# Kernel optimization log

Hardware: AMD Instinct MI355X
Metric: run time of the kernel (lower is better)

## Reference

```python
import jax, jax.numpy as jnp
import numpy as np

B, NP, K, E = 8, 4096, 1024, 262144   # graphs, nodes/graph, topk keep, edges
N = B * NP
EPS = 1e-5


def _glorot(k, fi, fo):
    lim = float(np.sqrt(6.0 / (fi + fo)))
    return jax.random.uniform(k, (fi, fo), jnp.float32, -lim, lim)


def setup_inputs() -> dict:
    key = jax.random.key(0)
    ks = jax.random.split(key, 16)
    pos = jax.random.normal(ks[0], (N, 3), jnp.float32)
    epg = E // B
    src = jax.random.randint(ks[1], (E,), 0, NP)
    dst = jax.random.randint(ks[2], (E,), 0, NP)
    off = jnp.repeat(jnp.arange(B) * NP, epg)   # edges stay within their graph
    edge_index = jnp.stack([src + off, dst + off]).astype(jnp.int32)
    batch = jnp.repeat(jnp.arange(B, dtype=jnp.int32), NP)
    inp = {"pos": pos, "edge_index": edge_index, "batch": batch,
           "p": jax.random.normal(ks[3], (3,), jnp.float32)}
    dims = [3, 64, 128, 128, 256, 512]
    for i in range(5):
        fi, fo = dims[i], dims[i + 1]
        inp[f"W{i+1}"] = _glorot(ks[4 + i], fi, fo)
        inp[f"b{i+1}"] = jnp.zeros((fo,), jnp.float32)
        inp[f"g{i+1}"] = jnp.ones((fo,), jnp.float32)
        inp[f"be{i+1}"] = jnp.zeros((fo,), jnp.float32)
    for i, (fi, fo) in enumerate([(512, 256), (256, 256), (256, 100)]):
        inp[f"fw{i+1}"] = _glorot(ks[9 + i], fi, fo)
        inp[f"fb{i+1}"] = jnp.zeros((fo,), jnp.float32)
    return inp


def _bn(x, g, b):
    # BatchNorm1d in training mode: batch stats over the node dim
    m = jnp.mean(x, 0)
    v = jnp.var(x, 0)
    return (x - m) * jax.lax.rsqrt(v + EPS) * g + b


def _gcn(x, src, dst, ew, W, bb, n):
    # GCNConv with add_self_loops=True, symmetric normalization.
    h = x @ W                                              # [n, out]
    deg = jax.ops.segment_sum(ew, dst, num_segments=n) + 1.0  # +1 self-loop
    dinv = jax.lax.rsqrt(deg)
    norm = dinv[src] * ew * dinv[dst]                      # masked edges -> 0
    agg = jax.ops.segment_sum(h[src] * norm[:, None], dst, num_segments=n)
    return agg + h * (dinv * dinv)[:, None] + bb           # self-loop term + bias


def _forward(pos, p, W1, b1, g1, be1, W2, b2, g2, be2, W3, b3, g3, be3,
             W4, b4, g4, be4, W5, b5, g5, be5, fw1, fb1, fw2, fb2, fw3, fb3,
             edge_index):
    # --- TopKPooling(ratio=1024): projection score, tanh, top-k per graph ---
    s = jnp.tanh(pos @ p / jnp.linalg.norm(p))             # [N]
    vals, idx = jax.lax.top_k(s.reshape(B, NP), K)         # [B,K]
    perm = (idx + (jnp.arange(B) * NP)[:, None]).reshape(-1)
    x = pos[perm] * vals.reshape(-1)[:, None]              # gate kept nodes
    Nn = B * K
    remap = jnp.full((N,), -1, jnp.int32).at[perm].set(jnp.arange(Nn, dtype=jnp.int32))
    src, dst = remap[edge_index[0]], remap[edge_index[1]]
    valid = (src >= 0) & (dst >= 0)
    ew = valid.astype(x.dtype)                             # 0-weight == removed edge
    src = jnp.where(valid, src, 0)
    dst = jnp.where(valid, dst, 0)
    for (W, bb, g, be) in ((W1, b1, g1, be1), (W2, b2, g2, be2),
                           (W3, b3, g3, be3), (W4, b4, g4, be4),
                           (W5, b5, g5, be5)):
        x = jax.nn.relu(_bn(_gcn(x, src, dst, ew, W, bb, Nn), g, be))
    # --- global sum pooling (torch_scatter default reduce='sum') ---
    batch_new = jnp.repeat(jnp.arange(B), K)
    x = jax.ops.segment_sum(x, batch_new, num_segments=B)  # [B,512]
    x = jax.nn.relu(x @ fw1 + fb1)
    x = jax.nn.relu(x @ fw2 + fb2)
    return jax.nn.log_softmax(x @ fw3 + fb3, axis=-1)      # [B,100]


def reference(pos, edge_index, batch, p, W1, b1, g1, be1, W2, b2, g2, be2,
              W3, b3, g3, be3, W4, b4, g4, be4, W5, b5, g5, be5,
              fw1, fb1, fw2, fb2, fw3, fb3):
    del batch  # graph ids are the fixed contiguous layout encoded in B, NP, K
    return _forward(pos, p, W1, b1, g1, be1, W2, b2, g2, be2, W3, b3, g3, be3,
                    W4, b4, g4, be4, W5, b5, g5, be5,
                    fw1, fb1, fw2, fb2, fw3, fb3, edge_index)
```

## Files before the change

kernel.cpp:

```cpp
#include <hip/hip_runtime.h>
#include <math.h>

#define NTOT 32768
#define NPG  4096
#define BGR  8
#define KK   1024
#define NN   8192
#define NE   262144

typedef __attribute__((ext_vector_type(8))) short bf16x8;
typedef __attribute__((ext_vector_type(4))) float f32x4;

static __device__ __forceinline__ unsigned short f2bf(float f) {
    unsigned u = __float_as_uint(f);
    return (unsigned short)((u + 0x7fffu + ((u >> 16) & 1u)) >> 16);
}
static __device__ __forceinline__ float bf2f(unsigned short b) {
    return __uint_as_float(((unsigned)b) << 16);
}

__global__ void k_init(int* remap, int* deg, int* cursor) {
    int i = blockIdx.x * blockDim.x + threadIdx.x;
    if (i < NTOT) remap[i] = -1;
    if (i < NN) { deg[i] = 0; cursor[i] = 0; }
}

__global__ __launch_bounds__(1024) void k_topk2(const float* __restrict__ pos,
                                                const float* __restrict__ p,
                                                int* __restrict__ remap,
                                                float* __restrict__ x0f,
                                                unsigned short* __restrict__ Ab0) {
    __shared__ unsigned skey[NPG];
    __shared__ float sval[NPG];
    __shared__ int hist[256];
    __shared__ int Sarr[256];
    __shared__ int wsum[16];
    __shared__ int s_bin, s_above;

    const int g = blockIdx.x, tid = threadIdx.x;
    const int lane = tid & 63, wid = tid >> 6;
    const float p0 = p[0], p1 = p[1], p2 = p[2];
    const float invn = 1.0f / sqrtf(p0 * p0 + p1 * p1 + p2 * p2);

    for (int i = tid; i < NPG; i += 1024) {
        const float* pp = pos + (size_t)(g * NPG + i) * 3;
        float s = tanhf((pp[0] * p0 + pp[1] * p1 + pp[2] * p2) * invn);
        sval[i] = s;
        unsigned b = __float_as_uint(s);
        skey[i] = (b & 0x80000000u) ? ~b : (b | 0x80000000u);
    }
    __syncthreads();

    unsigned prefix = 0;
    int needed = KK;
    for (int r = 0; r < 4; ++r) {
        const int sh = 24 - 8 * r;
        if (tid < 256) hist[tid] = 0;
        __syncthreads();
        for (int i = tid; i < NPG; i += 1024) {
            unsigned k = skey[i];
            bool act = (r == 0) || ((k >> (sh + 8)) == prefix);
            if (act) atomicAdd(&hist[(k >> sh) & 255u], 1);
        }
        __syncthreads();
        if (wid == 0) {
            int h0 = hist[4 * lane + 0], h1 = hist[4 * lane + 1];
            int h2 = hist[4 * lane + 2], h3 = hist[4 * lane + 3];
            int l3 = h3, l2 = h2 + l3, l1 = h1 + l2, l0 = h0 + l1;
            int t = l0;
            for (int off = 1; off < 64; off <<= 1) {
                int n = __shfl_down(t, off, 64);
                if (lane + off < 64) t += n;
            }
            int hi = t - l0;
            Sarr[4 * lane + 0] = l0 + hi;
            Sarr[4 * lane + 1] = l1 + hi;
            Sarr[4 * lane + 2] = l2 + hi;
            Sarr[4 * lane + 3] = l3 + hi;
        }
        __syncthreads();
        if (tid < 256) {
            int Sb = Sarr[tid];
            int Sb1 = (tid < 255) ? Sarr[tid + 1] : 0;
            if (Sb >= needed && Sb1 < needed) { s_bin = tid; s_above = Sb1; }
        }
        __syncthreads();
        needed -= s_above;
        prefix = (prefix << 8) | (unsigned)s_bin;
        __syncthreads();
    }
    const unsigned Tkey = prefix;
    const int needTies = needed;

    int tiebase = 0, keepbase = 0;
    for (int c = 0; c < 4; ++c) {
        const int i = c * 1024 + tid;
        const unsigned k = skey[i];
        const int tie = (k == Tkey) ? 1 : 0;
        int v = tie;
        for (int off = 1; off < 64; off <<= 1) {
            int n = __shfl_up(v, off, 64);
            if (lane >= off) v += n;
        }
        if (lane == 63) wsum[wid] = v;
        __syncthreads();
        if (wid == 0) {
            int w = (lane < 16) ? wsum[lane] : 0;
            for (int off = 1; off < 16; off <<= 1) {
                int n = __shfl_up(w, off, 64);
                if (lane >= off) w += n;
            }
            if (lane < 16) wsum[lane] = w;
        }
        __syncthreads();
        const int trank = tiebase + v + (wid > 0 ? wsum[wid - 1] : 0) - tie;
        const int ttot = wsum[15];
        const int keep = (k > Tkey) || (tie && trank < needTies);
        __syncthreads();
        int u = keep;
        for (int off = 1; off < 64; off <<= 1) {
            int n = __shfl_up(u, off, 64);
            if (lane >= off) u += n;
        }
        if (lane == 63) wsum[wid] = u;
        __syncthreads();
        if (wid == 0) {
            int w = (lane < 16) ? wsum[lane] : 0;
            for (int off = 1; off < 16; off <<= 1) {
                int n = __shfl_up(w, off, 64);
                if (lane >= off) w += n;
            }
            if (lane < 16) wsum[lane] = w;
        }
        __syncthreads();
        const int kincl = u + (wid > 0 ? wsum[wid - 1] : 0);
        const int ktot = wsum[15];
        if (keep) {
            int nn = g * KK + keepbase + kincl - 1;
            remap[g * NPG + i] = nn;
            float val = sval[i];
            const float* pp = pos + (size_t)(g * NPG + i) * 3;
            float v0 = pp[0] * val, v1 = pp[1] * val, v2 = pp[2] * val;
            x0f[(size_t)nn * 3 + 0] = v0;
            x0f[(size_t)nn * 3 + 1] = v1;
            x0f[(size_t)nn * 3 + 2] = v2;
            unsigned short* rw = Ab0 + (size_t)nn * 32;
            ushort4 a = make_ushort4(f2bf(v0), f2bf(v1), f2bf(v2), 0);
            ushort4 z = make_ushort4(0, 0, 0, 0);
            *(ushort4*)(rw) = a;
#pragma unroll
            for (int t = 1; t < 8; ++t) *(ushort4*)(rw + 4 * t) = z;
        }
        tiebase += ttot;
        keepbase += ktot;
        __syncthreads();
    }
}

__global__ void k_deg(const int* __restrict__ ei, const int* __restrict__ remap,
                      int* __restrict__ deg) {
    int e = blockIdx.x * blockDim.x + threadIdx.x;
    if (e >= NE) return;
    int s = remap[ei[e]];
    int d = remap[ei[NE + e]];
    if (s >= 0 && d >= 0) atomicAdd(&deg[d], 1);
}

__global__ __launch_bounds__(1024) void k_scan(const int* __restrict__ deg,
                                               int* __restrict__ rowptr) {
    __shared__ int part[1024];
    const int tid = threadIdx.x;
    const int base = tid * 8;
    int loc[8];
    int s = 0;
#pragma unroll
    for (int i = 0; i < 8; ++i) { loc[i] = s; s += deg[base + i]; }
    part[tid] = s;
    __syncthreads();
    for (int off = 1; off < 1024; off <<= 1) {
        int v = (tid >= off) ? part[tid - off] : 0;
        __syncthreads();
        part[tid] += v;
        __syncthreads();
    }
    int pre = (tid > 0) ? part[tid - 1] : 0;
#pragma unroll
    for (int i = 0; i < 8; ++i) rowptr[base + i] = pre + loc[i];
    if (tid == 1023) rowptr[NN] = pre + s;
}

__global__ void k_place2(const int* __restrict__ ei, const int* __restrict__ remap,
                         const int* __restrict__ deg, const int* __restrict__ rowptr,
                         int* __restrict__ cursor, int* __restrict__ col,
                         float* __restrict__ ew) {
    int e = blockIdx.x * blockDim.x + threadIdx.x;
    if (e >= NE) return;
    int s = remap[ei[e]];
    int d = remap[ei[NE + e]];
    if (s >= 0 && d >= 0) {
        int pos = rowptr[d] + atomicAdd(&cursor[d], 1);
        col[pos] = s;
        ew[pos] = rsqrtf((float)(deg[s] + 1)) * rsqrtf((float)(deg[d] + 1));
    }
}

__global__ void k_wt_all(const float* __restrict__ w0, const float* __restrict__ w1,
                         const float* __restrict__ w2, const float* __restrict__ w3,
                         const float* __restrict__ w4,
                         unsigned short* __restrict__ t0, unsigned short* __restrict__ t1,
                         unsigned short* __restrict__ t2, unsigned short* __restrict__ t3,
                         unsigned short* __restrict__ t4) {
    int i = blockIdx.x * blockDim.x + threadIdx.x;
    const float* W; unsigned short* T; int Kd, Nc, Kpad, base;
    if (i < 2048)        { W = w0; T = t0; Kd = 3;   Nc = 64;  Kpad = 32;  base = 0; }
    else if (i < 10240)  { W = w1; T = t1; Kd = 64;  Nc = 128; Kpad = 64;  base = 2048; }
    else if (i < 26624)  { W = w2; T = t2; Kd = 128; Nc = 128; Kpad = 128; base = 10240; }
    else if (i < 59392)  { W = w3; T = t3; Kd = 128; Nc = 256; Kpad = 128; base = 26624; }
    else if (i < 190464) { W = w4; T = t4; Kd = 256; Nc = 512; Kpad = 256; base = 59392; }
    else return;
    int j = i - base;
    int n = j / Kpad, k = j - n * Kpad;
    float v = (k < Kd) ? W[(size_t)k * Nc + n] : 0.0f;
    T[j] = f2bf(v);
}

__global__ __launch_bounds__(256) void k_mm2(const unsigned short* __restrict__ Ab,
                                             const float* __restrict__ Yin,
                                             const float* __restrict__ scale,
                                             const float* __restrict__ shift,
                                             const unsigned short* __restrict__ WT,
                                             unsigned short* __restrict__ Hb,
                                             int Kd, int Nc) {
    const int lane = threadIdx.x & 63, wid = threadIdx.x >> 6;
    const int bm = blockIdx.x * 64 + (wid >> 1) * 32;
    const int bn = blockIdx.y * 64 + (wid & 1) * 32;
    const int fr = lane & 15;
    const int ko = (lane >> 4) << 3;
    const int row0 = bm + fr;
    const unsigned short* B0 = WT + (size_t)(bn + fr) * Kd + ko;
    const size_t strA = (size_t)16 * Kd;
    f32x4 acc00 = {0,0,0,0}, acc01 = {0,0,0,0}, acc10 = {0,0,0,0}, acc11 = {0,0,0,0};
    for (int k0 = 0; k0 < Kd; k0 += 32) {
        bf16x8 a0, a1;
        if (Yin) {
            const int cc = ko + k0;
            const float4 sc0 = *(const float4*)&scale[cc];
            const float4 sc1 = *(const float4*)&scale[cc + 4];
            const float4 sh0 = *(const float4*)&shift[cc];
            const float4 sh1 = *(const float4*)&shift[cc + 4];
            const float* y0 = Yin + (size_t)row0 * Kd + cc;
            const float* y1 = y0 + strA;
#pragma unroll
            for (int h = 0; h < 2; ++h) {
                const float* yy = h ? y1 : y0;
                float4 u = *(const float4*)yy;
                float4 v = *(const float4*)(yy + 4);
                float r0 = fmaxf(u.x * sc0.x + sh0.x, 0.0f);
                float r1 = fmaxf(u.y * sc0.y + sh0.y, 0.0f);
                float r2 = fmaxf(u.z * sc0.z + sh0.z, 0.0f);
                float r3 = fmaxf(u.w * sc0.w + sh0.w, 0.0f);
                float r4 = fmaxf(v.x * sc1.x + sh1.x, 0.0f);
                float r5 = fmaxf(v.y * sc1.y + sh1.y, 0.0f);
                float r6 = fmaxf(v.z * sc1.z + sh1.z, 0.0f);
                float r7 = fmaxf(v.w * sc1.w + sh1.w, 0.0f);
                bf16x8 a;
                a[0] = (short)f2bf(r0); a[1] = (short)f2bf(r1);
                a[2] = (short)f2bf(r2); a[3] = (short)f2bf(r3);
                a[4] = (short)f2bf(r4); a[5] = (short)f2bf(r5);
                a[6] = (short)f2bf(r6); a[7] = (short)f2bf(r7);
                if (h) a1 = a; else a0 = a;
            }
        } else {
            const unsigned short* A0 = Ab + (size_t)row0 * Kd + ko + k0;
            a0 = *(const bf16x8*)A0;
            a1 = *(const bf16x8*)(A0 + strA);
        }
        bf16x8 b0 = *(const bf16x8*)(B0 + k0);
        bf16x8 b1 = *(const bf16x8*)(B0 + strA + k0);
        acc00 = __builtin_amdgcn_mfma_f32_16x16x32_bf16(b0, a0, acc00, 0, 0, 0);
        acc01 = __builtin_amdgcn_mfma_f32_16x16x32_bf16(b1, a0, acc01, 0, 0, 0);
        acc10 = __builtin_amdgcn_mfma_f32_16x16x32_bf16(b0, a1, acc10, 0, 0, 0);
        acc11 = __builtin_amdgcn_mfma_f32_16x16x32_bf16(b1, a1, acc11, 0, 0, 0);
    }
    const int r = lane & 15;
    const int c4 = (lane >> 4) << 2;
#pragma unroll
    for (int tm = 0; tm < 2; ++tm) {
        const int row = bm + tm * 16 + r;
        const size_t basep = (size_t)row * Nc;
        const f32x4 aL = tm ? acc10 : acc00;
        const f32x4 aR = tm ? acc11 : acc01;
#pragma unroll
        for (int tn = 0; tn < 2; ++tn) {
            const f32x4 a = tn ? aR : aL;
            const int c = bn + tn * 16 + c4;
            *(ushort4*)&Hb[basep + c] = make_ushort4(f2bf(a[0]), f2bf(a[1]),
                                                     f2bf(a[2]), f2bf(a[3]));
        }
    }
}

#define BM 64
#define BNT 64
#define BKT 16
__global__ __launch_bounds__(256) void k_mm(const float* __restrict__ A,
                                            const float* __restrict__ W,
                                            float* __restrict__ H, int Kd, int Nc) {
    __shared__ float As[BM][BKT + 1];
    __shared__ float Bs[BKT][BNT + 1];
    const int bm = blockIdx.x * BM;
    const int bn = blockIdx.y * BNT;
    const int tid = threadIdx.x;
    const int tx = tid & 15, ty = tid >> 4;
    float acc[4][4] = {};
    for (int k0 = 0; k0 < Kd; k0 += BKT) {
        for (int t = 0; t < 4; ++t) {
            int i = tid + t * 256;
            int m = i >> 4, k = i & 15;
            As[m][k] = (k0 + k < Kd) ? A[(size_t)(bm + m) * Kd + k0 + k] : 0.0f;
        }
        for (int t = 0; t < 4; ++t) {
            int i = tid + t * 256;
            int k = i >> 6, n = i & 63;
            Bs[k][n] = (k0 + k < Kd) ? W[(size_t)(k0 + k) * Nc + bn + n] : 0.0f;
        }
        __syncthreads();
        for (int k = 0; k < BKT; ++k) {
            float a[4], b[4];
#pragma unroll
            for (int i = 0; i < 4; ++i) a[i] = As[ty * 4 + i][k];
#pragma unroll
            for (int j = 0; j < 4; ++j) b[j] = Bs[k][tx * 4 + j];
#pragma unroll
            for (int i = 0; i < 4; ++i)
#pragma unroll
                for (int j = 0; j < 4; ++j) acc[i][j] += a[i] * b[j];
        }
        __syncthreads();
    }
#pragma unroll
    for (int i = 0; i < 4; ++i)
        *(float4*)&H[(size_t)(bm + ty * 4 + i) * Nc + bn + tx * 4] =
            make_float4(acc[i][0], acc[i][1], acc[i][2], acc[i][3]);
}

#define BN1_ROWS 16
#define BN1_CHUNKS (NN / BN1_ROWS)
__global__ __launch_bounds__(256) void k_gfuse(const unsigned short* __restrict__ Hb,
                                               const float* __restrict__ Hf,
                                               const int* __restrict__ rowptr,
                                               const int* __restrict__ col,
                                               const float* __restrict__ ew,
                                               const int* __restrict__ deg,
                                               const float* __restrict__ bias,
                                               float* __restrict__ Y,
                                               float* __restrict__ psum,
                                               float* __restrict__ psq, int Nc) {
    __shared__ float4 ls[256], lq[256];
    const int CHB = (Nc < 128) ? Nc : 128;
    const int CB = Nc / CHB;
    const int chunk = blockIdx.x / CB;
    const int cb = blockIdx.x - chunk * CB;
    const int QPB = CHB >> 2;
    const int tid = threadIdx.x;
    const int q = tid & (QPB - 1);
    const int rg = tid / QPB;
    const int NRG = 256 / QPB;
    const int RPT = BN1_ROWS / NRG;
    const int c = cb * CHB + (q << 2);
    const float4 b4 = *(const float4*)&bias[c];
    float4 s4 = make_float4(0, 0, 0, 0), q4 = make_float4(0, 0, 0, 0);
    for (int rr = 0; rr < RPT; ++rr) {
        const int n = chunk * BN1_ROWS + rg * RPT + rr;
        const int j0 = rowptr[n], j1 = rowptr[n + 1];
        const float inv = 1.0f / (float)(deg[n] + 1);
        float4 acc;
        if (Hb) {
            ushort4 hv = *(const ushort4*)&Hb[(size_t)n * Nc + c];
            acc = make_float4(bf2f(hv.x), bf2f(hv.y), bf2f(hv.z), bf2f(hv.w));
        } else {
            acc = *(const float4*)&Hf[(size_t)n * Nc + c];
        }
        acc.x = acc.x * inv + b4.x;
        acc.y = acc.y * inv + b4.y;
        acc.z = acc.z * inv + b4.z;
        acc.w = acc.w * inv + b4.w;
        if (Hb) {
            for (int j = j0; j < j1; ++j) {
                const float w = ew[j];
                ushort4 hv = *(const ushort4*)&Hb[(size_t)col[j] * Nc + c];
                acc.x += bf2f(hv.x) * w; acc.y += bf2f(hv.y) * w;
                acc.z += bf2f(hv.z) * w; acc.w += bf2f(hv.w) * w;
            }
        } else {
            for (int j = j0; j < j1; ++j) {
                const float w = ew[j];
                const float4 hv = *(const float4*)&Hf[(size_t)col[j] * Nc + c];
                acc.x += hv.x * w; acc.y += hv.y * w; acc.z += hv.z * w; acc.w += hv.w * w;
            }
        }
        *(float4*)&Y[(size_t)n * Nc + c] = acc;
        s4.x += acc.x; s4.y += acc.y; s4.z += acc.z; s4.w += acc.w;
        q4.x += acc.x * acc.x; q4.y += acc.y * acc.y;
        q4.z += acc.z * acc.z; q4.w += acc.w * acc.w;
    }
    ls[tid] = s4; lq[tid] = q4;
    __syncthreads();
    for (int st = 128; st >= QPB; st >>= 1) {
        if (tid < st) {
            float4 a = ls[tid], b = ls[tid + st];
            ls[tid] = make_float4(a.x + b.x, a.y + b.y, a.z + b.z, a.w + b.w);
            float4 e = lq[tid], f = lq[tid + st];
            lq[tid] = make_float4(e.x + f.x, e.y + f.y, e.z + f.z, e.w + f.w);
        }
        __syncthreads();
    }
    if (tid < QPB) {
        *(float4*)&psum[(size_t)chunk * Nc + c] = ls[tid];
        *(float4*)&psq[(size_t)chunk * Nc + c] = lq[tid];
    }
}

__global__ __launch_bounds__(256) void k_bn2p(const float* __restrict__ psum,
                                              const float* __restrict__ psq,
                                              const float* __restrict__ g,
                                              const float* __restrict__ be,
                                              float* __restrict__ scale,
                                              float* __restrict__ shift, int Nc) {
    __shared__ float ss[256], sq[256];
    const int c = blockIdx.x;
    const int t = threadIdx.x;
    float s = 0.0f, q = 0.0f;
    for (int b = t; b < BN1_CHUNKS; b += 256) {
        s += psum[(size_t)b * Nc + c];
        q += psq[(size_t)b * Nc + c];
    }
    ss[t] = s; sq[t] = q;
    __syncthreads();
    for (int st = 128; st > 0; st >>= 1) {
        if (t < st) { ss[t] += ss[t + st]; sq[t] += sq[t + st]; }
        __syncthreads();
    }
    if (t == 0) {
        double mean = (double)ss[0] / 8192.0;
        double var = (double)sq[0] / 8192.0 - mean * mean;
        float sc = (float)((double)g[c] / sqrt(var + 1e-5));
        scale[c] = sc;
        shift[c] = be[c] - (float)mean * sc;
    }
}

__global__ void k_bnapply(float* x, const float* __restrict__ scale,
                          const float* __restrict__ shift, int Nc) {
    int i = blockIdx.x * blockDim.x + threadIdx.x;
    int c4 = i & ((Nc >> 2) - 1);
    float4 v = ((const float4*)x)[i];
    float4 sc = ((const float4*)scale)[c4];
    float4 sh = ((const float4*)shift)[c4];
    v.x = fmaxf(v.x * sc.x + sh.x, 0.0f);
    v.y = fmaxf(v.y * sc.y + sh.y, 0.0f);
    v.z = fmaxf(v.z * sc.z + sh.z, 0.0f);
    v.w = fmaxf(v.w * sc.w + sh.w, 0.0f);
    ((float4*)x)[i] = v;
}

#define PR 32
__global__ __launch_bounds__(256) void k_pool_af(const float* __restrict__ Y,
                                                 const float* __restrict__ scale,
                                                 const float* __restrict__ shift,
                                                 float* __restrict__ part) {
    __shared__ float4 red[128];
    const int g = blockIdx.x >> 5;
    const int rs = blockIdx.x & 31;
    const int half = threadIdx.x >> 7;
    const int q = threadIdx.x & 127;
    const float4 sc = *(const float4*)&scale[4 * q];
    const float4 sh = *(const float4*)&shift[4 * q];
    const float* xp = Y + (size_t)(g * KK + rs * PR + half * 16) * 512 + 4 * q;
    float4 s = make_float4(0, 0, 0, 0);
#pragma unroll
    for (int rr = 0; rr < 16; ++rr) {
        float4 v = *(const float4*)(xp + (size_t)rr * 512);
        s.x += fmaxf(v.x * sc.x + sh.x, 0.0f);
        s.y += fmaxf(v.y * sc.y + sh.y, 0.0f);
        s.z += fmaxf(v.z * sc.z + sh.z, 0.0f);
        s.w += fmaxf(v.w * sc.w + sh.w, 0.0f);
    }
    if (half == 1) red[q] = s;
    __syncthreads();
    if (half == 0) {
        float4 t = red[q];
        s.x += t.x; s.y += t.y; s.z += t.z; s.w += t.w;
        *(float4*)&part[(size_t)blockIdx.x * 512 + 4 * q] = s;
    }
}

__global__ __launch_bounds__(256) void k_pool(const float* __restrict__ x, float* pooled) {
    __shared__ float red[4][64];
    int g = blockIdx.x >> 3;
    int c0 = (blockIdx.x & 7) * 64;
    int c = threadIdx.x & 63;
    int rp = threadIdx.x >> 6;
    float s = 0;
    for (int r = rp; r < KK; r += 4)
        s += x[(size_t)(g * KK + r) * 512 + c0 + c];
    red[rp][c] = s;
    __syncthreads();
    if (rp == 0)
        pooled[g * 512 + c0 + c] = red[0][c] + red[1][c] + red[2][c] + red[3][c];
}

__global__ __launch_bounds__(256) void k_fc1(const float* __restrict__ part,
                                             const float* __restrict__ fw1,
                                             const float* __restrict__ fb1,
                                             float* __restrict__ t1, int nparts) {
    __shared__ float pooled[512];
    const int g = blockIdx.x, tid = threadIdx.x;
    for (int c = tid; c < 512; c += 256) {
        float s = 0;
        for (int i = 0; i < nparts; ++i) s += part[(size_t)(g * nparts + i) * 512 + c];
        pooled[c] = s;
    }
    __syncthreads();
    float acc = fb1[tid];
    for (int k = 0; k < 512; ++k) acc += pooled[k] * fw1[k * 256 + tid];
    t1[g * 256 + tid] = acc > 0.0f ? acc : 0.0f;
}

__global__ void k_fc(const float* __restrict__ in, const float* __restrict__ W,
                     const float* __restrict__ bias, float* out, int fi, int fo) {
    __shared__ float row[512];
    int g = blockIdx.x, tid = threadIdx.x;
    for (int k = tid; k < fi; k += blockDim.x) row[k] = in[g * fi + k];
    __syncthreads();
    if (tid < fo) {
        float acc = bias[tid];
        for (int k = 0; k < fi; ++k) acc += row[k] * W[k * fo + tid];
        out[g * fo + tid] = acc > 0.0f ? acc : 0.0f;
    }
}

__global__ __launch_bounds__(256) void k_fc23(const float* __restrict__ t1,
                                              const float* __restrict__ fw2,
                                              const float* __restrict__ fb2,
                                              const float* __restrict__ fw3,
                                              const float* __restrict__ fb3,
                                              float* __restrict__ out) {
    __shared__ float row[256];
    __shared__ float t2s[256];
    __shared__ float red[256];
    __shared__ float logits[100];
    const int g = blockIdx.x, tid = threadIdx.x;
    row[tid] = t1[g * 256 + tid];
    __syncthreads();
    float acc = fb2[tid];
    for (int k = 0; k < 256; ++k) acc += row[k] * fw2[k * 256 + tid];
    t2s[tid] = acc > 0.0f ? acc : 0.0f;
    __syncthreads();
    float v = -INFINITY;
    if (tid < 100) {
        float a3 = fb3[tid];
        for (int k = 0; k < 256; ++k) a3 += t2s[k] * fw3[k * 100 + tid];
        logits[tid] = a3;
        v = a3;
    }
    red[tid] = v;
    __syncthreads();
    for (int s = 128; s > 0; s >>= 1) {
        if (tid < s) red[tid] = fmaxf(red[tid], red[tid + s]);
        __syncthreads();
    }
    float mx = red[0];
    __syncthreads();
    red[tid] = (tid < 100) ? expf(logits[tid] - mx) : 0.0f;
    __syncthreads();
    for (int s = 128; s > 0; s >>= 1) {
        if (tid < s) red[tid] += red[tid + s];
        __syncthreads();
    }
    float lse = logf(red[0]);
    if (tid < 100) out[g * 100 + tid] = logits[tid] - mx - lse;
}

extern "C" void kernel_launch(void* const* d_in, const int* in_sizes, int n_in,
                              void* d_out, int out_size, void* d_ws, size_t ws_size,
                              hipStream_t stream) {
    const float* pos = (const float*)d_in[0];
    const int* ei = (const int*)d_in[1];
    const float* p = (const float*)d_in[3];
    const float *W[5], *bb[5], *gg[5], *be[5];
    for (int i = 0; i < 5; ++i) {
        W[i]  = (const float*)d_in[4 + 4 * i];
        bb[i] = (const float*)d_in[5 + 4 * i];
        gg[i] = (const float*)d_in[6 + 4 * i];
        be[i] = (const float*)d_in[7 + 4 * i];
    }
    const float* fw1 = (const float*)d_in[24]; const float* fb1 = (const float*)d_in[25];
    const float* fw2 = (const float*)d_in[26]; const float* fb2 = (const float*)d_in[27];
    const float* fw3 = (const float*)d_in[28]; const float* fb3 = (const float*)d_in[29];
    float* out = (float*)d_out;

    const int fins[5]  = {3, 64, 128, 128, 256};
    const int kpads[5] = {32, 64, 128, 128, 256};
    const int fouts[5] = {64, 128, 128, 256, 512};

    size_t off = 0;
    char* base = (char*)d_ws;
    auto alloc = [&](size_t bytes) { char* q = base + off; off += (bytes + 255) & ~(size_t)255; return q; };

    float* Y      = (float*)alloc((size_t)NN * 512 * 4);
    float* Hf     = (float*)alloc((size_t)NN * 512 * 4);
    int*   remap  = (int*)alloc((size_t)NTOT * 4);
    int*   deg    = (int*)alloc(NN * 4);
    int*   cursor = (int*)alloc(NN * 4);
    int*   rowptr = (int*)alloc((NN + 1) * 4);
    int*   ecol   = (int*)alloc((size_t)NE * 4);
    float* ew     = (float*)alloc((size_t)NE * 4);
    float* psum   = (float*)alloc((size_t)BN1_CHUNKS * 512 * 4);
    float* psq    = (float*)alloc((size_t)BN1_CHUNKS * 512 * 4);
    float* scale  = (float*)alloc(512 * 4);
    float* shift  = (float*)alloc(512 * 4);
    float* pooled = (float*)alloc(8 * 512 * 4);
    float* t1     = (float*)alloc(8 * 256 * 4);
    unsigned short* Ab0 = (unsigned short*)alloc((size_t)NN * 32 * 2);
    float* part   = (float*)alloc((size_t)256 * 512 * 4);
    unsigned short* WT[5];
    for (int l = 0; l < 5; ++l) WT[l] = (unsigned short*)alloc((size_t)fouts[l] * kpads[l] * 2);
    unsigned short* Hb = (unsigned short*)Hf;
    const bool mfma = (ws_size >= off);

    k_init<<<NTOT / 256, 256, 0, stream>>>(remap, deg, cursor);
    k_topk2<<<BGR, 1024, 0, stream>>>(pos, p, remap, Y, Ab0);
    k_deg<<<NE / 256, 256, 0, stream>>>(ei, remap, deg);
    k_scan<<<1, 1024, 0, stream>>>(deg, rowptr);
    k_place2<<<NE / 256, 256, 0, stream>>>(ei, remap, deg, rowptr, cursor, ecol, ew);

    if (mfma) {
        k_wt_all<<<(190464 + 255) / 256, 256, 0, stream>>>(W[0], W[1], W[2], W[3], W[4],
                                                           WT[0], WT[1], WT[2], WT[3], WT[4]);
        for (int l = 0; l < 5; ++l) {
            int fo = fouts[l];
            dim3 mg(NN / 64, fo / 64);
            if (l == 0)
                k_mm2<<<mg, 256, 0, stream>>>(Ab0, nullptr, nullptr, nullptr,
                                              WT[l], Hb, kpads[l], fo);
            else
                k_mm2<<<mg, 256, 0, stream>>>(nullptr, Y, scale, shift,
                                              WT[l], Hb, kpads[l], fo);
            int cbs = (fo < 128) ? 1 : fo / 128;
            k_gfuse<<<BN1_CHUNKS * cbs, 256, 0, stream>>>(Hb, nullptr, rowptr, ecol, ew,
                                                          deg, bb[l], Y, psum, psq, fo);
            k_bn2p<<<fo, 256, 0, stream>>>(psum, psq, gg[l], be[l], scale, shift, fo);
        }
        k_pool_af<<<256, 256, 0, stream>>>(Y, scale, shift, part);
        k_fc1<<<8, 256, 0, stream>>>(part, fw1, fb1, t1, 32);
        k_fc23<<<8, 256, 0, stream>>>(t1, fw2, fb2, fw3, fb3, out);
    } else {
        for (int l = 0; l < 5; ++l) {
            int fi = fins[l], fo = fouts[l];
            dim3 mg(NN / BM, fo / BNT);
            k_mm<<<mg, 256, 0, stream>>>(Y, W[l], Hf, fi, fo);
            int cbs = (fo < 128) ? 1 : fo / 128;
            k_gfuse<<<BN1_CHUNKS * cbs, 256, 0, stream>>>(nullptr, Hf, rowptr, ecol, ew,
                                                          deg, bb[l], Y, psum, psq, fo);
            k_bn2p<<<fo, 256, 0, stream>>>(psum, psq, gg[l], be[l], scale, shift, fo);
            k_bnapply<<<(NN * fo) / 1024, 256, 0, stream>>>(Y, scale, shift, fo);
        }
        k_pool<<<64, 256, 0, stream>>>(Y, pooled);
        k_fc<<<8, 256, 0, stream>>>(pooled, fw1, fb1, t1, 512, 256);
        k_fc23<<<8, 256, 0, stream>>>(t1, fw2, fb2, fw3, fb3, out);
    }
}
```

Measured before the change: 218.2 us.

## Fold init into topk kernel and split FC head across more blocks

Removes the separate init kernel by having the top-k kernel zero deg/cursor and write -1 remap entries for dropped nodes. The FC head, formerly two 8-block kernels with long serial K loops, becomes three kernels that split the input dimension across a 2D grid and write partial sums. This cuts one launch and raises parallelism in the tail, at the cost of one extra launch and scratch buffers for the partials. The BN/ReLU-to-bf16 code in the matmul is restyled inline and should compile the same.

```diff
diff --git a/kernel.cpp b/kernel.cpp
--- a/kernel.cpp
+++ b/kernel.cpp
@@ -19,17 +19,13 @@
     return __uint_as_float(((unsigned)b) << 16);
 }
 
-__global__ void k_init(int* remap, int* deg, int* cursor) {
-    int i = blockIdx.x * blockDim.x + threadIdx.x;
-    if (i < NTOT) remap[i] = -1;
-    if (i < NN) { deg[i] = 0; cursor[i] = 0; }
-}
-
 __global__ __launch_bounds__(1024) void k_topk2(const float* __restrict__ pos,
                                                 const float* __restrict__ p,
                                                 int* __restrict__ remap,
                                                 float* __restrict__ x0f,
-                                                unsigned short* __restrict__ Ab0) {
+                                                unsigned short* __restrict__ Ab0,
+                                                int* __restrict__ deg,
+                                                int* __restrict__ cursor) {
     __shared__ unsigned skey[NPG];
     __shared__ float sval[NPG];
     __shared__ int hist[256];
@@ -39,6 +35,8 @@
 
     const int g = blockIdx.x, tid = threadIdx.x;
     const int lane = tid & 63, wid = tid >> 6;
+    deg[g * KK + tid] = 0;
+    cursor[g * KK + tid] = 0;
     const float p0 = p[0], p1 = p[1], p2 = p[2];
     const float invn = 1.0f / sqrtf(p0 * p0 + p1 * p1 + p2 * p2);
 
@@ -150,6 +148,8 @@
             *(ushort4*)(rw) = a;
 #pragma unroll
             for (int t = 1; t < 8; ++t) *(ushort4*)(rw + 4 * t) = z;
+        } else {
+            remap[g * NPG + i] = -1;
         }
         tiebase += ttot;
         keepbase += ktot;
@@ -255,19 +255,15 @@
                 const float* yy = h ? y1 : y0;
                 float4 u = *(const float4*)yy;
                 float4 v = *(const float4*)(yy + 4);
-                float r0 = fmaxf(u.x * sc0.x + sh0.x, 0.0f);
-                float r1 = fmaxf(u.y * sc0.y + sh0.y, 0.0f);
-                float r2 = fmaxf(u.z * sc0.z + sh0.z, 0.0f);
-                float r3 = fmaxf(u.w * sc0.w + sh0.w, 0.0f);
-                float r4 = fmaxf(v.x * sc1.x + sh1.x, 0.0f);
-                float r5 = fmaxf(v.y * sc1.y + sh1.y, 0.0f);
-                float r6 = fmaxf(v.z * sc1.z + sh1.z, 0.0f);
-                float r7 = fmaxf(v.w * sc1.w + sh1.w, 0.0f);
                 bf16x8 a;
-                a[0] = (short)f2bf(r0); a[1] = (short)f2bf(r1);
-                a[2] = (short)f2bf(r2); a[3] = (short)f2bf(r3);
-                a[4] = (short)f2bf(r4); a[5] = (short)f2bf(r5);
-                a[6] = (short)f2bf(r6); a[7] = (short)f2bf(r7);
+                a[0] = (short)f2bf(fmaxf(u.x * sc0.x + sh0.x, 0.0f));
+                a[1] = (short)f2bf(fmaxf(u.y * sc0.y + sh0.y, 0.0f));
+                a[2] = (short)f2bf(fmaxf(u.z * sc0.z + sh0.z, 0.0f));
+                a[3] = (short)f2bf(fmaxf(u.w * sc0.w + sh0.w, 0.0f));
+                a[4] = (short)f2bf(fmaxf(v.x * sc1.x + sh1.x, 0.0f));
+                a[5] = (short)f2bf(fmaxf(v.y * sc1.y + sh1.y, 0.0f));
+                a[6] = (short)f2bf(fmaxf(v.z * sc1.z + sh1.z, 0.0f));
+                a[7] = (short)f2bf(fmaxf(v.w * sc1.w + sh1.w, 0.0f));
                 if (h) a1 = a; else a0 = a;
             }
         } else {
@@ -510,21 +506,85 @@
         pooled[g * 512 + c0 + c] = red[0][c] + red[1][c] + red[2][c] + red[3][c];
 }
 
-__global__ __launch_bounds__(256) void k_fc1(const float* __restrict__ part,
-                                             const float* __restrict__ fw1,
-                                             const float* __restrict__ fb1,
-                                             float* __restrict__ t1, int nparts) {
-    __shared__ float pooled[512];
+__global__ __launch_bounds__(256) void k_fc1s(const float* __restrict__ part,
+                                              const float* __restrict__ fw1,
+                                              float* __restrict__ part2) {
+    __shared__ float pooled_s[32];
+    __shared__ float red[256];
+    const int g = blockIdx.x, s = blockIdx.y, tid = threadIdx.x;
+    const int j = tid & 31;
+    const int i = tid >> 5;
+    float p = 0;
+    for (int a = i; a < 32; a += 8)
+        p += part[(size_t)(g * 32 + a) * 512 + 32 * s + j];
+    red[tid] = p;
+    __syncthreads();
+    if (tid < 32) {
+        float t = red[tid];
+        for (int i2 = 1; i2 < 8; ++i2) t += red[i2 * 32 + tid];
+        pooled_s[tid] = t;
+    }
+    __syncthreads();
+    float acc = 0;
+    const float* wp = fw1 + (size_t)(32 * s) * 256 + tid;
+#pragma unroll
+    for (int k = 0; k < 32; ++k) acc += pooled_s[k] * wp[k * 256];
+    part2[(size_t)(g * 16 + s) * 256 + tid] = acc;
+}
+
+__global__ __launch_bounds__(256) void k_fc2s(const float* __restrict__ part2,
+                                              const float* __restrict__ fb1,
+                                              const float* __restrict__ fw2,
+                                              float* __restrict__ part3) {
+    __shared__ float t1s[256];
+    const int g = blockIdx.x, s = blockIdx.y, tid = threadIdx.x;
+    float a1 = fb1[tid];
+    for (int i = 0; i < 16; ++i) a1 += part2[(size_t)(g * 16 + i) * 256 + tid];
+    t1s[tid] = fmaxf(a1, 0.0f);
+    __syncthreads();
+    float acc = 0;
+    const float* wp = fw2 + (size_t)(32 * s) * 256 + tid;
+#pragma unroll
+    for (int k = 0; k < 32; ++k) acc += t1s[32 * s + k] * wp[k * 256];
+    part3[(size_t)(g * 8 + s) * 256 + tid] = acc;
+}
+
+__global__ __launch_bounds__(256) void k_fc3f(const float* __restrict__ part3,
+                                              const float* __restrict__ fb2,
+                                              const float* __restrict__ fw3,
+                                              const float* __restrict__ fb3,
+                                              float* __restrict__ out) {
+    __shared__ float t2s[256];
+    __shared__ float red[256];
+    __shared__ float logits[100];
     const int g = blockIdx.x, tid = threadIdx.x;
-    for (int c = tid; c < 512; c += 256) {
-        float s = 0;
-        for (int i = 0; i < nparts; ++i) s += part[(size_t)(g * nparts + i) * 512 + c];
-        pooled[c] = s;
-    }
-    __syncthreads();
-    float acc = fb1[tid];
-    for (int k = 0; k < 512; ++k) acc += pooled[k] * fw1[k * 256 + tid];
-    t1[g * 256 + tid] = acc > 0.0f ? acc : 0.0f;
+    float a2 = fb2[tid];
+    for (int i = 0; i < 8; ++i) a2 += part3[(size_t)(g * 8 + i) * 256 + tid];
+    t2s[tid] = fmaxf(a2, 0.0f);
+    __syncthreads();
+    float v = -INFINITY;
+    if (tid < 100) {
+        float a3 = fb3[tid];
+        for (int k = 0; k < 256; ++k) a3 += t2s[k] * fw3[k * 100 + tid];
+        logits[tid] = a3;
+        v = a3;
+    }
+    red[tid] = v;
+    __syncthreads();
+    for (int s = 128; s > 0; s >>= 1) {
+        if (tid < s) red[tid] = fmaxf(red[tid], red[tid + s]);
+        __syncthreads();
+    }
+    float mx = red[0];
+    __syncthreads();
+    red[tid] = (tid < 100) ? expf(logits[tid] - mx) : 0.0f;
+    __syncthreads();
+    for (int s = 128; s > 0; s >>= 1) {
+        if (tid < s) red[tid] += red[tid + s];
+        __syncthreads();
+    }
+    float lse = logf(red[0]);
+    if (tid < 100) out[g * 100 + tid] = logits[tid] - mx - lse;
 }
 
 __global__ void k_fc(const float* __restrict__ in, const float* __restrict__ W,
@@ -624,13 +684,14 @@
     float* t1     = (float*)alloc(8 * 256 * 4);
     unsigned short* Ab0 = (unsigned short*)alloc((size_t)NN * 32 * 2);
     float* part   = (float*)alloc((size_t)256 * 512 * 4);
+    float* part2  = (float*)alloc((size_t)8 * 16 * 256 * 4);
+    float* part3  = (float*)alloc((size_t)8 * 8 * 256 * 4);
     unsigned short* WT[5];
     for (int l = 0; l < 5; ++l) WT[l] = (unsigned short*)alloc((size_t)fouts[l] * kpads[l] * 2);
     unsigned short* Hb = (unsigned short*)Hf;
     const bool mfma = (ws_size >= off);
 
-    k_init<<<NTOT / 256, 256, 0, stream>>>(remap, deg, cursor);
-    k_topk2<<<BGR, 1024, 0, stream>>>(pos, p, remap, Y, Ab0);
+    k_topk2<<<BGR, 1024, 0, stream>>>(pos, p, remap, Y, Ab0, deg, cursor);
     k_deg<<<NE / 256, 256, 0, stream>>>(ei, remap, deg);
     k_scan<<<1, 1024, 0, stream>>>(deg, rowptr);
     k_place2<<<NE / 256, 256, 0, stream>>>(ei, remap, deg, rowptr, cursor, ecol, ew);
@@ -653,8 +714,9 @@
             k_bn2p<<<fo, 256, 0, stream>>>(psum, psq, gg[l], be[l], scale, shift, fo);
         }
         k_pool_af<<<256, 256, 0, stream>>>(Y, scale, shift, part);
-        k_fc1<<<8, 256, 0, stream>>>(part, fw1, fb1, t1, 32);
-        k_fc23<<<8, 256, 0, stream>>>(t1, fw2, fb2, fw3, fb3, out);
+        k_fc1s<<<dim3(8, 16), 256, 0, stream>>>(part, fw1, part2);
+        k_fc2s<<<dim3(8, 8), 256, 0, stream>>>(part2, fb1, fw2, part3);
+        k_fc3f<<<8, 256, 0, stream>>>(part3, fb2, fw3, fb3, out);
     } else {
         for (int l = 0; l < 5; ++l) {
             int fi = fins[l], fo = fouts[l];
```

New measurement: 184.1 us. 1.19x faster.
